# Optimization experiments

Measured on AMD Instinct MI355X. Metric: run time of the kernel, lower is better.

## Reference

```python
import jax, jax.numpy as jnp
import numpy as np
import math

B, H, S, D = 2, 16, 2048, 64

def setup_inputs() -> dict:
    key = jax.random.key(0)
    kq, kk, kv, km = jax.random.split(key, 4)
    query = jax.random.normal(kq, (B, H, S, D), dtype=jnp.float32)
    k_ = jax.random.normal(kk, (B, H, S, D), dtype=jnp.float32)
    value = jax.random.normal(kv, (B, H, S, D), dtype=jnp.float32)
    mask = jax.random.randint(km, (B, 1, 1, S), 0, 2, dtype=jnp.int32)
    return {"query": query, "key": k_, "value": value, "mask": mask}

def reference(query, key, value, mask):
    # scores: [B,H,S,S] = QK^T / sqrt(D)
    scale = 1.0 / math.sqrt(query.shape[-1])
    scores = jnp.einsum('bhqd,bhkd->bhqk', query, key) * scale
    # masked_fill(mask == 0, -1e9); mask broadcasts [B,1,1,S] -> [B,H,S,S]
    scores = jnp.where(mask == 0, jnp.float32(-1e9), scores)
    p_attn = jax.nn.softmax(scores, axis=-1)
    out = jnp.einsum('bhqk,bhkd->bhqd', p_attn, value)
    return (out, p_attn)
```

## Files before the change

kernel.cpp:

```cpp
#include <hip/hip_runtime.h>
#include <cstdint>
#include <cstddef>


typedef float f32x4 __attribute__((ext_vector_type(4)));
typedef short s16x8 __attribute__((ext_vector_type(8)));
typedef unsigned int u32;

#define S_LEN 2048
#define D_DIM 64
#define NKT   32
#define QSCALE 0.18033688011112042f

__device__ __forceinline__ unsigned short f2bf(float f) {
  unsigned u = __builtin_bit_cast(unsigned, f);
  u += 0x7FFFu + ((u >> 16) & 1u);
  return (unsigned short)(u >> 16);
}

__device__ __forceinline__ f32x4 mfma16(s16x8 a, s16x8 b, f32x4 c) {
  return __builtin_amdgcn_mfma_f32_16x16x32_bf16(a, b, c, 0, 0, 0);
}

__device__ __forceinline__ void gl_lds16(const void* g, void* l) {
  __builtin_amdgcn_global_load_lds(
      (const __attribute__((address_space(1))) u32*)g,
      (__attribute__((address_space(3))) u32*)l, 16, 0, 0);
}

__global__ void prep_kv(const float* __restrict__ Kg, const float* __restrict__ Vg,
                        unsigned short* __restrict__ kb, unsigned short* __restrict__ vb) {
  __shared__ float tv[64 * 65];
  const int kt = blockIdx.x, bh = blockIdx.y, tid = threadIdx.x;
  const int r = tid >> 2, c0 = (tid & 3) << 4;
  if (blockIdx.z == 0) {
    const float* src = Kg + (((size_t)bh * S_LEN) + kt * 64 + r) * D_DIM + c0;
    f32x4 f0 = *(const f32x4*)(src);
    f32x4 f1 = *(const f32x4*)(src + 4);
    f32x4 f2 = *(const f32x4*)(src + 8);
    f32x4 f3 = *(const f32x4*)(src + 12);
    s16x8 h0, h1;
#pragma unroll
    for (int j = 0; j < 4; j++) {
      h0[j] = (short)f2bf(f0[j]); h0[j + 4] = (short)f2bf(f1[j]);
      h1[j] = (short)f2bf(f2[j]); h1[j + 4] = (short)f2bf(f3[j]);
    }
    char* dst = (char*)(kb + ((size_t)bh * 32 + kt) * 4096);
    const int swz = (r & 7) << 4;
    *(s16x8*)(dst + (r << 7) + (((c0 << 1) + 0)  ^ swz)) = h0;
    *(s16x8*)(dst + (r << 7) + (((c0 << 1) + 16) ^ swz)) = h1;
  } else {
    const float* src = Vg + (((size_t)bh * S_LEN) + kt * 64 + r) * D_DIM + c0;
#pragma unroll
    for (int j = 0; j < 4; j++)
      *(f32x4*)(tv + r * 65 + c0 + j * 4) = *(const f32x4*)(src + j * 4);
    __syncthreads();
    const int d = tid >> 2, k0 = (tid & 3) << 4;
    s16x8 h0, h1;
#pragma unroll
    for (int j = 0; j < 8; j++) {
      h0[j] = (short)f2bf(tv[(k0 + j) * 65 + d]);
      h1[j] = (short)f2bf(tv[(k0 + 8 + j) * 65 + d]);
    }
    char* dst = (char*)(vb + ((size_t)bh * 32 + kt) * 4096);
    const int swz = (d & 7) << 4;
    *(s16x8*)(dst + (d << 7) + (((k0 << 1) + 0)  ^ swz)) = h0;
    *(s16x8*)(dst + (d << 7) + (((k0 << 1) + 16) ^ swz)) = h1;
  }
}


__global__ __launch_bounds__(512, 4) void attn_main(
    const float* __restrict__ Qg, const unsigned short* __restrict__ Kb,
    const unsigned short* __restrict__ Vb, const int* __restrict__ Mg,
    float* __restrict__ Og, float* __restrict__ Pg)
{
  __shared__ __align__(16) short s_kv[8][4096];
  __shared__ __align__(16) short s_p[8][1024];

  const int tid = threadIdx.x;
  const int w = tid >> 6, l = tid & 63, lo = l & 15, hi = l >> 4;
  const int wg = blockIdx.x;
  const int bh = (wg & 7) * 4 + ((wg >> 3) >> 4);
  const int qt = (wg >> 3) & 15;
  const int b = bh >> 4;
  const int ph = wg & 31;

  unsigned* mbuild = (unsigned*)s_p;
  if (tid < 64) mbuild[tid] = 0u;
  __syncthreads();
  {
    const int4 mv = *(const int4*)(Mg + b * S_LEN + tid * 4);
    unsigned nib = (mv.x ? 1u : 0u) | (mv.y ? 2u : 0u) |
                   (mv.z ? 4u : 0u) | (mv.w ? 8u : 0u);
    atomicOr(&mbuild[tid >> 3], nib << ((tid & 7) * 4));
  }
  __syncthreads();
  const unsigned mword = mbuild[l];
  __syncthreads();

  const size_t bhS = (size_t)bh * S_LEN;
  const int q0w = qt * 128 + w * 16;

  const float* qsrc = Qg + (bhS + q0w + lo) * D_DIM + hi * 8;
  s16x8 bq0, bq1;
  {
    f32x4 a0 = *(const f32x4*)(qsrc);
    f32x4 a1 = *(const f32x4*)(qsrc + 4);
    f32x4 c0 = *(const f32x4*)(qsrc + 32);
    f32x4 c1 = *(const f32x4*)(qsrc + 36);
#pragma unroll
    for (int j = 0; j < 4; j++) {
      bq0[j]     = (short)f2bf(a0[j] * QSCALE);
      bq0[j + 4] = (short)f2bf(a1[j] * QSCALE);
      bq1[j]     = (short)f2bf(c0[j] * QSCALE);
      bq1[j + 4] = (short)f2bf(c1[j] * QSCALE);
    }
  }

  const char* ktile = (const char*)(Kb + bhS * D_DIM);
  const char* vtile = (const char*)(Vb + bhS * D_DIM);
  char* base = (char*)s_kv;
  char* pb  = (char*)s_p[w];
  const int swz = (lo & 7) << 4;
  const int hs  = hi << 2;

  gl_lds16(ktile + ((0 + ph) & 31) * 8192 + tid * 16, base + 0 * 8192 + tid * 16);
  gl_lds16(ktile + ((1 + ph) & 31) * 8192 + tid * 16, base + 1 * 8192 + tid * 16);
  gl_lds16(ktile + ((2 + ph) & 31) * 8192 + tid * 16, base + 2 * 8192 + tid * 16);
  gl_lds16(ktile + ((3 + ph) & 31) * 8192 + tid * 16, base + 3 * 8192 + tid * 16);

  float lacc[4] = {0.f, 0.f, 0.f, 0.f};
  for (int j = 0; j < 8; j++) {
    const int h = j & 1;
    asm volatile("s_waitcnt vmcnt(0)" ::: "memory");
    __builtin_amdgcn_s_barrier();
    __builtin_amdgcn_sched_barrier(0);
    if (j < 7) {
      const int tb = 4 * j + 4;
      char* dst = base + (h ^ 1) * 32768;
      gl_lds16(ktile + ((tb + 0 + ph) & 31) * 8192 + tid * 16, dst + 0 * 8192 + tid * 16);
      gl_lds16(ktile + ((tb + 1 + ph) & 31) * 8192 + tid * 16, dst + 1 * 8192 + tid * 16);
      gl_lds16(ktile + ((tb + 2 + ph) & 31) * 8192 + tid * 16, dst + 2 * 8192 + tid * 16);
      gl_lds16(ktile + ((tb + 3 + ph) & 31) * 8192 + tid * 16, dst + 3 * 8192 + tid * 16);
    }
#pragma unroll
    for (int t2 = 0; t2 < 4; t2++) {
      const int t = (4 * j + t2 + ph) & 31;
      const char* kc = base + h * 32768 + t2 * 8192;
      f32x4 acc[4] = {};
      __builtin_amdgcn_s_setprio(1);
#pragma unroll
      for (int nn = 0; nn < 4; nn++) {
        const int rb = (nn * 16 + lo) << 7;
        s16x8 ka0 = *(const s16x8*)(kc + rb + ((0 + hi * 16) ^ swz));
        s16x8 ka1 = *(const s16x8*)(kc + rb + ((64 + hi * 16) ^ swz));
        acc[nn] = mfma16(ka0, bq0, acc[nn]);
        acc[nn] = mfma16(ka1, bq1, acc[nn]);
      }
      __builtin_amdgcn_s_setprio(0);
      const unsigned w0 = (unsigned)__shfl((int)mword, 2 * t);
      const unsigned w1 = (unsigned)__shfl((int)mword, 2 * t + 1);
#pragma unroll
      for (int nn = 0; nn < 4; nn++) {
        const unsigned m4 = (((nn & 2) ? w1 : w0) >> (((nn & 1) << 4) + hs)) & 0xF;
#pragma unroll
        for (int r = 0; r < 4; r++) {
          const float e = exp2f(acc[nn][r]);
          lacc[nn] += ((m4 >> r) & 1) ? e : 0.0f;
        }
      }
    }
  }
  float lsum = (lacc[0] + lacc[1]) + (lacc[2] + lacc[3]);
  lsum += __shfl_xor(lsum, 16, 64);
  lsum += __shfl_xor(lsum, 32, 64);
  const float inv = 1.0f / lsum;

  __syncthreads();

  char* ldsk = base;
  char* ldsv = base + 32768;
  gl_lds16(ktile + ((0 + ph) & 31) * 8192 + tid * 16, ldsk + 0 * 8192 + tid * 16);
  gl_lds16(ktile + ((1 + ph) & 31) * 8192 + tid * 16, ldsk + 1 * 8192 + tid * 16);
  gl_lds16(vtile + ((0 + ph) & 31) * 8192 + tid * 16, ldsv + 0 * 8192 + tid * 16);
  gl_lds16(vtile + ((1 + ph) & 31) * 8192 + tid * 16, ldsv + 1 * 8192 + tid * 16);

  f32x4 oacc[4] = {};
  for (int j = 0; j < 16; j++) {
    const int h = j & 1;
    if (j == 0) asm volatile("s_waitcnt vmcnt(0)" ::: "memory");
    else        asm volatile("s_waitcnt vmcnt(8)" ::: "memory");
    __builtin_amdgcn_s_barrier();
    __builtin_amdgcn_sched_barrier(0);
    if (j < 15) {
      gl_lds16(ktile + ((2 * j + 2 + ph) & 31) * 8192 + tid * 16,
               ldsk + (2 * (h ^ 1)) * 8192 + tid * 16);
      gl_lds16(ktile + ((2 * j + 3 + ph) & 31) * 8192 + tid * 16,
               ldsk + (2 * (h ^ 1) + 1) * 8192 + tid * 16);
      gl_lds16(vtile + ((2 * j + 2 + ph) & 31) * 8192 + tid * 16,
               ldsv + (2 * (h ^ 1)) * 8192 + tid * 16);
      gl_lds16(vtile + ((2 * j + 3 + ph) & 31) * 8192 + tid * 16,
               ldsv + (2 * (h ^ 1) + 1) * 8192 + tid * 16);
    }
#pragma unroll
    for (int t2 = 0; t2 < 2; t2++) {
      const int t = (2 * j + t2 + ph) & 31;
      const char* kc = ldsk + (2 * h + t2) * 8192;
      const char* vc = ldsv + (2 * h + t2) * 8192;

      f32x4 acc[4] = {};
      __builtin_amdgcn_s_setprio(1);
#pragma unroll
      for (int nn = 0; nn < 4; nn++) {
        const int rb = (nn * 16 + lo) << 7;
        s16x8 ka0 = *(const s16x8*)(kc + rb + ((0 + hi * 16) ^ swz));
        s16x8 ka1 = *(const s16x8*)(kc + rb + ((64 + hi * 16) ^ swz));
        acc[nn] = mfma16(ka0, bq0, acc[nn]);
        acc[nn] = mfma16(ka1, bq1, acc[nn]);
      }
      __builtin_amdgcn_s_setprio(0);
      const unsigned w0 = (unsigned)__shfl((int)mword, 2 * t);
      const unsigned w1 = (unsigned)__shfl((int)mword, 2 * t + 1);
      const int colb = t * 64;
      float* prow = Pg + (bhS + q0w + lo) * S_LEN + colb;
#pragma unroll
      for (int nn = 0; nn < 4; nn++) {
        const unsigned m4 = (((nn & 2) ? w1 : w0) >> (((nn & 1) << 4) + hs)) & 0xF;
        f32x4 p;
#pragma unroll
        for (int r = 0; r < 4; r++) {
          const float e = exp2f(acc[nn][r]) * inv;
          p[r] = ((m4 >> r) & 1) ? e : 0.0f;
        }
        *(f32x4*)(prow + nn * 16 + hi * 4) = p;
        unsigned d0, d1;
        asm("v_cvt_pk_bf16_f32 %0, %1, %2" : "=v"(d0) : "v"(p[0]), "v"(p[1]));
        asm("v_cvt_pk_bf16_f32 %0, %1, %2" : "=v"(d1) : "v"(p[2]), "v"(p[3]));
        *(unsigned long long*)(pb + (lo << 7) + ((nn * 32 + hi * 8) ^ swz)) =
            ((unsigned long long)d1 << 32) | d0;
      }
      __builtin_amdgcn_s_setprio(1);
#pragma unroll
      for (int kk2 = 0; kk2 < 2; kk2++) {
        s16x8 bp = *(const s16x8*)(pb + (lo << 7) + ((kk2 * 64 + hi * 16) ^ swz));
#pragma unroll
        for (int dd = 0; dd < 4; dd++) {
          s16x8 va = *(const s16x8*)(vc + ((dd * 16 + lo) << 7) +
                                     ((kk2 * 64 + hi * 16) ^ swz));
          oacc[dd] = mfma16(va, bp, oacc[dd]);
        }
      }
      __builtin_amdgcn_s_setprio(0);
    }
  }
#pragma unroll
  for (int dd = 0; dd < 4; dd++)
    *(f32x4*)(Og + (bhS + q0w + lo) * D_DIM + dd * 16 + hi * 4) = oacc[dd];
}


__device__ __forceinline__ void stage_k(const float* __restrict__ g, char* lb, int tid) {
  const int kr = tid >> 2;
  const int c0 = (tid & 3) << 4;
  const f32x4* src = (const f32x4*)(g + kr * D_DIM + c0);
  f32x4 f0 = src[0], f1 = src[1], f2 = src[2], f3 = src[3];
  s16x8 h0, h1;
#pragma unroll
  for (int j = 0; j < 4; j++) {
    h0[j] = (short)f2bf(f0[j]); h0[j + 4] = (short)f2bf(f1[j]);
    h1[j] = (short)f2bf(f2[j]); h1[j + 4] = (short)f2bf(f3[j]);
  }
  const int base = kr << 7;
  const int swz = (kr & 7) << 4;
  *(s16x8*)(lb + base + (((c0 << 1) + 0) ^ swz)) = h0;
  *(s16x8*)(lb + base + (((c0 << 1) + 16) ^ swz)) = h1;
}

__device__ __forceinline__ void stage_v(const float* __restrict__ g, char* lb, int tid) {
  const int k0 = (tid >> 3) << 1;
  const int c0 = (tid & 7) << 3;
  const f32x4* s0 = (const f32x4*)(g + k0 * D_DIM + c0);
  const f32x4* s1 = (const f32x4*)(g + (k0 + 1) * D_DIM + c0);
  f32x4 a0 = s0[0], a1 = s0[1];
  f32x4 b0 = s1[0], b1 = s1[1];
  const int kc = (k0 >> 3) & 7;
  const int kb2 = (k0 & 7) << 1;
#pragma unroll
  for (int j = 0; j < 8; j++) {
    float fa = (j < 4) ? a0[j & 3] : a1[j & 3];
    float fb = (j < 4) ? b0[j & 3] : b1[j & 3];
    unsigned u = (unsigned)f2bf(fa) | ((unsigned)f2bf(fb) << 16);
    const int d = c0 + j;
    const int off = (d << 7) + (((kc ^ j ^ (d >> 3)) & 7) << 4) + kb2;
    *(unsigned*)(lb + off) = u;
  }
}

__global__ __launch_bounds__(256, 4) void attn_fwd(
    const float* __restrict__ Qg, const float* __restrict__ Kg,
    const float* __restrict__ Vg, const int* __restrict__ Mg,
    float* __restrict__ Og, float* __restrict__ Pg)
{
  __shared__ __align__(16) float s_bias[S_LEN];
  __shared__ __align__(16) short s_k[64 * 64];
  __shared__ __align__(16) short s_v[64 * 64];
  __shared__ __align__(16) short s_p[4 * 16 * 64];

  const int tid = threadIdx.x;
  const int w = tid >> 6, l = tid & 63, lo = l & 15, hi = l >> 4;
  const int bh = blockIdx.x, qt = blockIdx.y, b = bh >> 4;

  for (int i = tid; i < S_LEN; i += 256)
    s_bias[i] = Mg[b * S_LEN + i] ? 0.0f : -INFINITY;

  const int q0 = qt * 64 + w * 16;
  const float* qptr = Qg + ((size_t)bh * S_LEN + q0 + lo) * D_DIM + hi * 8;
  s16x8 aq[2];
#pragma unroll
  for (int kk = 0; kk < 2; kk++) {
    f32x4 v0 = *(const f32x4*)(qptr + kk * 32);
    f32x4 v1 = *(const f32x4*)(qptr + kk * 32 + 4);
#pragma unroll
    for (int j = 0; j < 4; j++) {
      aq[kk][j] = (short)f2bf(v0[j] * QSCALE);
      aq[kk][j + 4] = (short)f2bf(v1[j] * QSCALE);
    }
  }
  char* kb = (char*)s_k;
  char* vb = (char*)s_v;
  char* pb = (char*)s_p + (w << 11);
  const size_t bhS = (size_t)bh * S_LEN;
  __syncthreads();

  float lsum[4] = {0.f, 0.f, 0.f, 0.f};
  for (int kt = 0; kt < NKT; kt++) {
    stage_k(Kg + (bhS + kt * 64) * D_DIM, kb, tid);
    __syncthreads();
    f32x4 acc[4] = {};
#pragma unroll
    for (int kk = 0; kk < 2; kk++)
#pragma unroll
      for (int nn = 0; nn < 4; nn++) {
        const int row = nn * 16 + lo;
        s16x8 bk = *(const s16x8*)(kb + (row << 7) +
                     ((kk * 64 + hi * 16) ^ ((row & 7) << 4)));
        acc[nn] = mfma16(aq[kk], bk, acc[nn]);
      }
    const int colb = kt * 64;
#pragma unroll
    for (int nn = 0; nn < 4; nn++) {
      const float bias = s_bias[colb + nn * 16 + lo];
#pragma unroll
      for (int r = 0; r < 4; r++)
        lsum[r] += exp2f(acc[nn][r] + bias);
    }
    __syncthreads();
  }
#pragma unroll
  for (int r = 0; r < 4; r++)
#pragma unroll
    for (int off = 1; off < 16; off <<= 1)
      lsum[r] += __shfl_xor(lsum[r], off, 64);
  float inv[4];
#pragma unroll
  for (int r = 0; r < 4; r++) inv[r] = 1.0f / lsum[r];

  f32x4 oacc[4] = {};
  const int qd0 = q0 + hi * 4;
  for (int kt = 0; kt < NKT; kt++) {
    stage_k(Kg + (bhS + kt * 64) * D_DIM, kb, tid);
    stage_v(Vg + (bhS + kt * 64) * D_DIM, vb, tid);
    __syncthreads();
    f32x4 acc[4] = {};
#pragma unroll
    for (int kk = 0; kk < 2; kk++)
#pragma unroll
      for (int nn = 0; nn < 4; nn++) {
        const int row = nn * 16 + lo;
        s16x8 bk = *(const s16x8*)(kb + (row << 7) +
                     ((kk * 64 + hi * 16) ^ ((row & 7) << 4)));
        acc[nn] = mfma16(aq[kk], bk, acc[nn]);
      }
    const int colb = kt * 64;
#pragma unroll
    for (int nn = 0; nn < 4; nn++) {
      const int col = colb + nn * 16 + lo;
      const float bias = s_bias[col];
#pragma unroll
      for (int r = 0; r < 4; r++) {
        const float p = exp2f(acc[nn][r] + bias) * inv[r];
        Pg[(bhS + (size_t)(qd0 + r)) * S_LEN + col] = p;
        const int prow = hi * 4 + r;
        *(unsigned short*)(pb + (prow << 7) +
            ((((nn * 16 + lo) << 1)) ^ ((prow & 7) << 4))) = f2bf(p);
      }
    }
#pragma unroll
    for (int kk2 = 0; kk2 < 2; kk2++) {
      s16x8 ap = *(const s16x8*)(pb + (lo << 7) +
                   ((kk2 * 64 + hi * 16) ^ ((lo & 7) << 4)));
#pragma unroll
      for (int dd = 0; dd < 4; dd++) {
        const int d = dd * 16 + lo;
        const int chunk = ((kk2 * 4 + hi) ^ (d & 7) ^ (d >> 3)) & 7;
        s16x8 bv = *(const s16x8*)(vb + (d << 7) + (chunk << 4));
        oacc[dd] = mfma16(ap, bv, oacc[dd]);
      }
    }
    __syncthreads();
  }
#pragma unroll
  for (int dd = 0; dd < 4; dd++)
#pragma unroll
    for (int r = 0; r < 4; r++)
      Og[(bhS + (size_t)(qd0 + r)) * D_DIM + dd * 16 + lo] = oacc[dd][r];
}

extern "C" void kernel_launch(void* const* d_in, const int* in_sizes, int n_in,
                              void* d_out, int out_size, void* d_ws, size_t ws_size,
                              hipStream_t stream) {
  const float* Q = (const float*)d_in[0];
  const float* K = (const float*)d_in[1];
  const float* V = (const float*)d_in[2];
  const int*   M = (const int*)d_in[3];
  float* out = (float*)d_out;
  float* P = out + (size_t)2 * 16 * 2048 * 64;

  const size_t elems = (size_t)2 * 16 * 2048 * 64;
  if (ws_size >= elems * 2 * sizeof(unsigned short)) {
    unsigned short* kb = (unsigned short*)d_ws;
    unsigned short* vb = kb + elems;
    prep_kv<<<dim3(32, 32, 2), 256, 0, stream>>>(K, V, kb, vb);
    attn_main<<<dim3(512), 512, 0, stream>>>(Q, kb, vb, M, out, P);
  } else {
    attn_fwd<<<dim3(32, 32), dim3(256), 0, stream>>>(Q, K, V, M, out, P);
  }
}
```

Before: 171.3 us.

## Split attention kernel into row-sum pass and PV/probability pass

Splits the fused attention kernel into two launches. The first computes only the softmax denominators and writes the inverse sums to workspace. The second reloads them and computes the probabilities and PV output. This shrinks the LDS footprint and register pressure of the sum pass and lets each kernel be scheduled on its own, at the cost of an extra launch, recomputing the Q load and mask setup, and a small global round-trip for the inverse sums. It also needs a larger workspace; if that is not available the fallback kernel is used instead.

```diff
diff --git a/kernel.cpp b/kernel.cpp
--- a/kernel.cpp
+++ b/kernel.cpp
@@ -70,13 +70,12 @@
 }
 
 
-__global__ __launch_bounds__(512, 4) void attn_main(
+__global__ __launch_bounds__(512, 4) void attn_sums(
     const float* __restrict__ Qg, const unsigned short* __restrict__ Kb,
-    const unsigned short* __restrict__ Vb, const int* __restrict__ Mg,
-    float* __restrict__ Og, float* __restrict__ Pg)
+    const int* __restrict__ Mg, float* __restrict__ invb)
 {
-  __shared__ __align__(16) short s_kv[8][4096];
-  __shared__ __align__(16) short s_p[8][1024];
+  __shared__ __align__(16) short s_k[8][4096];
+  __shared__ unsigned s_m[64];
 
   const int tid = threadIdx.x;
   const int w = tid >> 6, l = tid & 63, lo = l & 15, hi = l >> 4;
@@ -86,18 +85,16 @@
   const int b = bh >> 4;
   const int ph = wg & 31;
 
-  unsigned* mbuild = (unsigned*)s_p;
-  if (tid < 64) mbuild[tid] = 0u;
+  if (tid < 64) s_m[tid] = 0u;
   __syncthreads();
   {
     const int4 mv = *(const int4*)(Mg + b * S_LEN + tid * 4);
     unsigned nib = (mv.x ? 1u : 0u) | (mv.y ? 2u : 0u) |
                    (mv.z ? 4u : 0u) | (mv.w ? 8u : 0u);
-    atomicOr(&mbuild[tid >> 3], nib << ((tid & 7) * 4));
-  }
-  __syncthreads();
-  const unsigned mword = mbuild[l];
-  __syncthreads();
+    atomicOr(&s_m[tid >> 3], nib << ((tid & 7) * 4));
+  }
+  __syncthreads();
+  const unsigned mword = s_m[l];
 
   const size_t bhS = (size_t)bh * S_LEN;
   const int q0w = qt * 128 + w * 16;
@@ -119,9 +116,7 @@
   }
 
   const char* ktile = (const char*)(Kb + bhS * D_DIM);
-  const char* vtile = (const char*)(Vb + bhS * D_DIM);
-  char* base = (char*)s_kv;
-  char* pb  = (char*)s_p[w];
+  char* base = (char*)s_k;
   const int swz = (lo & 7) << 4;
   const int hs  = hi << 2;
 
@@ -176,11 +171,67 @@
   lsum += __shfl_xor(lsum, 16, 64);
   lsum += __shfl_xor(lsum, 32, 64);
   const float inv = 1.0f / lsum;
-
-  __syncthreads();
-
-  char* ldsk = base;
-  char* ldsv = base + 32768;
+  if (l < 16) invb[bh * S_LEN + q0w + l] = inv;
+}
+
+
+__global__ __launch_bounds__(512, 4) void attn_pv(
+    const float* __restrict__ Qg, const unsigned short* __restrict__ Kb,
+    const unsigned short* __restrict__ Vb, const int* __restrict__ Mg,
+    const float* __restrict__ invb, float* __restrict__ Og, float* __restrict__ Pg)
+{
+  __shared__ __align__(16) short s_kv[8][4096];
+  __shared__ __align__(16) short s_p[8][1024];
+
+  const int tid = threadIdx.x;
+  const int w = tid >> 6, l = tid & 63, lo = l & 15, hi = l >> 4;
+  const int wg = blockIdx.x;
+  const int bh = (wg & 7) * 4 + ((wg >> 3) >> 4);
+  const int qt = (wg >> 3) & 15;
+  const int b = bh >> 4;
+  const int ph = wg & 31;
+
+  unsigned* mbuild = (unsigned*)s_p;
+  if (tid < 64) mbuild[tid] = 0u;
+  __syncthreads();
+  {
+    const int4 mv = *(const int4*)(Mg + b * S_LEN + tid * 4);
+    unsigned nib = (mv.x ? 1u : 0u) | (mv.y ? 2u : 0u) |
+                   (mv.z ? 4u : 0u) | (mv.w ? 8u : 0u);
+    atomicOr(&mbuild[tid >> 3], nib << ((tid & 7) * 4));
+  }
+  __syncthreads();
+  const unsigned mword = mbuild[l];
+  __syncthreads();
+
+  const size_t bhS = (size_t)bh * S_LEN;
+  const int q0w = qt * 128 + w * 16;
+
+  const float* qsrc = Qg + (bhS + q0w + lo) * D_DIM + hi * 8;
+  s16x8 bq0, bq1;
+  {
+    f32x4 a0 = *(const f32x4*)(qsrc);
+    f32x4 a1 = *(const f32x4*)(qsrc + 4);
+    f32x4 c0 = *(const f32x4*)(qsrc + 32);
+    f32x4 c1 = *(const f32x4*)(qsrc + 36);
+#pragma unroll
+    for (int j = 0; j < 4; j++) {
+      bq0[j]     = (short)f2bf(a0[j] * QSCALE);
+      bq0[j + 4] = (short)f2bf(a1[j] * QSCALE);
+      bq1[j]     = (short)f2bf(c0[j] * QSCALE);
+      bq1[j + 4] = (short)f2bf(c1[j] * QSCALE);
+    }
+  }
+  const float inv = invb[bh * S_LEN + q0w + lo];
+
+  const char* ktile = (const char*)(Kb + bhS * D_DIM);
+  const char* vtile = (const char*)(Vb + bhS * D_DIM);
+  char* ldsk = (char*)s_kv;
+  char* ldsv = (char*)s_kv + 32768;
+  char* pb  = (char*)s_p[w];
+  const int swz = (lo & 7) << 4;
+  const int hs  = hi << 2;
+
   gl_lds16(ktile + ((0 + ph) & 31) * 8192 + tid * 16, ldsk + 0 * 8192 + tid * 16);
   gl_lds16(ktile + ((1 + ph) & 31) * 8192 + tid * 16, ldsk + 1 * 8192 + tid * 16);
   gl_lds16(vtile + ((0 + ph) & 31) * 8192 + tid * 16, ldsv + 0 * 8192 + tid * 16);
@@ -428,11 +479,15 @@
   float* P = out + (size_t)2 * 16 * 2048 * 64;
 
   const size_t elems = (size_t)2 * 16 * 2048 * 64;
-  if (ws_size >= elems * 2 * sizeof(unsigned short)) {
+  const size_t need = elems * 2 * sizeof(unsigned short) + 
+                      (size_t)32 * S_LEN * sizeof(float);
+  if (ws_size >= need) {
     unsigned short* kb = (unsigned short*)d_ws;
     unsigned short* vb = kb + elems;
+    float* invb = (float*)(vb + elems);
     prep_kv<<<dim3(32, 32, 2), 256, 0, stream>>>(K, V, kb, vb);
-    attn_main<<<dim3(512), 512, 0, stream>>>(Q, kb, vb, M, out, P);
+    attn_sums<<<dim3(512), 512, 0, stream>>>(Q, kb, M, invb);
+    attn_pv<<<dim3(512), 512, 0, stream>>>(Q, kb, vb, M, invb, out, P);
   } else {
     attn_fwd<<<dim3(32, 32), dim3(256), 0, stream>>>(Q, K, V, M, out, P);
   }
```

New measurement: 210.3 us. 1.23x slower.
